# Performance work log

Measured on AMD Instinct MI355X. Metric: run time of the kernel, lower is better.

## Reference

```python
import jax, jax.numpy as jnp
import numpy as np

B = 4        # number of point clouds (equal-size contiguous batches)
P = 8192     # points per cloud
C_IN = 64
C_OUT = 64
K = 16       # kNN neighbors (includes the point itself, as in PyG knn)
EPS = 1e-5
NEG_SLOPE = 0.2


def setup_inputs() -> dict:
    key = jax.random.key(0)
    k1, k2, k3 = jax.random.split(key, 3)
    x = jax.random.normal(k1, (B * P, C_IN), dtype=jnp.float32)
    batch = jnp.repeat(jnp.arange(B, dtype=jnp.int64), P)  # sorted, equal sizes
    W = jax.random.normal(k2, (2 * C_IN, C_OUT), dtype=jnp.float32) * (1.0 / np.sqrt(2 * C_IN))
    b = jax.random.normal(k3, (C_OUT,), dtype=jnp.float32) * 0.01
    gamma = jnp.ones((C_OUT,), dtype=jnp.float32)
    beta = jnp.zeros((C_OUT,), dtype=jnp.float32)
    return {"x": x, "batch": batch, "W": W, "b": b, "gamma": gamma, "beta": beta}


def _edgeconv(x, W, b, gamma, beta):
    xb = x.reshape(B, P, C_IN)
    # per-cloud pairwise squared distances: [B, P, P]
    sq = jnp.sum(xb * xb, axis=-1)
    d = sq[:, :, None] + sq[:, None, :] - 2.0 * jnp.einsum("bpc,bqc->bpq", xb, xb)
    # k nearest neighbors (smallest distance, self included)
    _, idx = jax.lax.top_k(-d, K)                      # [B, P, K]
    xj = jax.vmap(lambda pts, ind: pts[ind])(xb, idx)  # [B, P, K, C_IN]
    xi = xb[:, :, None, :]
    e = jnp.concatenate([jnp.broadcast_to(xi, xj.shape), xj - xi], axis=-1)  # [B,P,K,2C]
    # edge MLP: Linear -> BatchNorm1d (training-mode batch stats over all edges) -> LeakyReLU
    h = jnp.einsum("bpke,eo->bpko", e, W) + b          # [B, P, K, C_OUT]
    hf = h.reshape(-1, C_OUT)
    mean = jnp.mean(hf, axis=0)
    var = jnp.mean(hf * hf, axis=0) - mean * mean      # biased variance (torch BN)
    hn = (h - mean) * jax.lax.rsqrt(var + EPS) * gamma + beta
    a = jnp.where(hn >= 0, hn, NEG_SLOPE * hn)
    # max aggregation over neighbors
    return jnp.max(a, axis=2).reshape(B * P, C_OUT)


def reference(x, batch, W, b, gamma, beta):
    # `batch` encodes B equal-size contiguous clouds; kNN is computed per cloud.
    return _edgeconv(x, W, b, gamma, beta)
```

## Files before the change

### kernel.cpp

```cpp
#include <hip/hip_runtime.h>
#include <cfloat>

#define BATCH 4
#define P 8192
#define C 64
#define KNN 16
#define NPTS (BATCH * P)
#define NEDGE (NPTS * KNN)
#define EPSV 1e-5f
#define SLOPE 0.2f
#define NQ 2
#define QCOLS (P / NQ)
#define NPART 4

typedef __attribute__((ext_vector_type(8))) short bf16x8;
typedef __attribute__((ext_vector_type(16))) float f32x16;


__device__ __forceinline__ unsigned short f2bf(float f) {
    unsigned u = __float_as_uint(f);
    u += 0x7FFFu + ((u >> 16) & 1u);
    return (unsigned short)(u >> 16);
}
__device__ __forceinline__ float bf2f(unsigned short s) {
    return __uint_as_float(((unsigned)s) << 16);
}

__global__ void prep_frag(const float* __restrict__ x, uint4* __restrict__ xfh,
                          uint4* __restrict__ xfm, uint4* __restrict__ xfl,
                          float* __restrict__ sq) {
    __shared__ float part[32][9];
    int tid = threadIdx.x;
    int ptl = tid >> 3, j8 = tid & 7;
    int g = blockIdx.x;
    int p = g * 32 + ptl;
    const float4* xp = (const float4*)(x + (size_t)p * C + j8 * 8);
    float4 a = xp[0], b = xp[1];
    float v[8] = {a.x, a.y, a.z, a.w, b.x, b.y, b.z, b.w};
    unsigned short hs[8], ms[8], ls[8];
    float ssum = 0.f;
#pragma unroll
    for (int e = 0; e < 8; ++e) {
        float xv = v[e];
        ssum = fmaf(xv, xv, ssum);
        unsigned short h = f2bf(xv);
        float r1 = xv - bf2f(h);
        unsigned short m = f2bf(r1);
        float r2 = r1 - bf2f(m);
        unsigned short l = f2bf(r2);
        hs[e] = h; ms[e] = m; ls[e] = l;
    }
    int dst = (g * 4 + (j8 >> 1)) * 64 + ptl + 32 * (j8 & 1);
    uint4 ph, pm, pl;
    ph.x = (unsigned)hs[0] | ((unsigned)hs[1] << 16);
    ph.y = (unsigned)hs[2] | ((unsigned)hs[3] << 16);
    ph.z = (unsigned)hs[4] | ((unsigned)hs[5] << 16);
    ph.w = (unsigned)hs[6] | ((unsigned)hs[7] << 16);
    pm.x = (unsigned)ms[0] | ((unsigned)ms[1] << 16);
    pm.y = (unsigned)ms[2] | ((unsigned)ms[3] << 16);
    pm.z = (unsigned)ms[4] | ((unsigned)ms[5] << 16);
    pm.w = (unsigned)ms[6] | ((unsigned)ms[7] << 16);
    pl.x = (unsigned)ls[0] | ((unsigned)ls[1] << 16);
    pl.y = (unsigned)ls[2] | ((unsigned)ls[3] << 16);
    pl.z = (unsigned)ls[4] | ((unsigned)ls[5] << 16);
    pl.w = (unsigned)ls[6] | ((unsigned)ls[7] << 16);
    xfh[dst] = ph; xfm[dst] = pm; xfl[dst] = pl;
    part[ptl][j8] = ssum;
    __syncthreads();
    if (j8 == 0) {
        float s = 0.f;
#pragma unroll
        for (int k = 0; k < 8; ++k) s += part[ptl][k];
        sq[p] = s;
    }
}

__global__ __launch_bounds__(256, 4) void knn_kernel(const uint4* __restrict__ xfh,
                                                     const uint4* __restrict__ xfm,
                                                     const uint4* __restrict__ xfl,
                                                     const float* __restrict__ sq,
                                                     float* __restrict__ pv,
                                                     int* __restrict__ pi) {
    __shared__ float          bufv[4 * 32 * 33];
    __shared__ unsigned short bufi[4 * 32 * 33];
    __shared__ int            idL [4 * 32 * 17];
    __shared__ int            cntL[4 * 32];
    __shared__ float          worstL[4 * 32];

    int tid = threadIdx.x;
    int b = blockIdx.x & 3;
    int t = blockIdx.x >> 2;
    int tile = t & 127;
    int half = t >> 7;
    int bglob = b * P;
    int r0 = tile * 64;
    int colbase = half * QCOLS;
    int w = tid >> 6, lane = tid & 63;
    int wr = w & 1, wc = w >> 1;

    float*          bufvW = bufv + w * (32 * 33);
    unsigned short* bufiW = bufi + w * (32 * 33);
    int*            idLW  = idL  + w * (32 * 17);
    int*            cntW  = cntL + w * 32;
    float*          worstW = worstL + w * 32;

    if (lane < 32) { cntW[lane] = 0; worstW[lane] = FLT_MAX; }

    int gA = ((bglob + r0) >> 5) + wr;
    bf16x8 Ah[4], Am[4], Al[4];
#pragma unroll
    for (int kk = 0; kk < 4; ++kk) {
        Ah[kk] = __builtin_bit_cast(bf16x8, xfh[(gA * 4 + kk) * 64 + lane]);
        Am[kk] = __builtin_bit_cast(bf16x8, xfm[(gA * 4 + kk) * 64 + lane]);
        Al[kk] = __builtin_bit_cast(bf16x8, xfl[(gA * 4 + kk) * 64 + lane]);
    }

    float tv[16];
    float worst = FLT_MAX;
#pragma unroll
    for (int j = 0; j < 16; ++j) tv[j] = FLT_MAX;

    int rlbase = 4 * (lane >> 5);
    int sub = lane & 31;
    int colq = wc * 32 + sub;

    for (int chunk = 0; chunk < QCOLS / 64; ++chunk) {
        int c0 = colbase + chunk * 64;
        int gB = ((bglob + c0) >> 5) + wc;
        float sc = sq[bglob + c0 + colq];

        f32x16 acc;
#pragma unroll
        for (int i = 0; i < 16; ++i) acc[i] = 0.f;

#pragma unroll
        for (int kk = 0; kk < 4; ++kk) {
            bf16x8 Bh = __builtin_bit_cast(bf16x8, xfh[(gB * 4 + kk) * 64 + lane]);
            bf16x8 Bm = __builtin_bit_cast(bf16x8, xfm[(gB * 4 + kk) * 64 + lane]);
            bf16x8 Bl = __builtin_bit_cast(bf16x8, xfl[(gB * 4 + kk) * 64 + lane]);
            acc = __builtin_amdgcn_mfma_f32_32x32x16_bf16(Ah[kk], Bh, acc, 0, 0, 0);
            acc = __builtin_amdgcn_mfma_f32_32x32x16_bf16(Am[kk], Bh, acc, 0, 0, 0);
            acc = __builtin_amdgcn_mfma_f32_32x32x16_bf16(Al[kk], Bh, acc, 0, 0, 0);
            acc = __builtin_amdgcn_mfma_f32_32x32x16_bf16(Ah[kk], Bm, acc, 0, 0, 0);
            acc = __builtin_amdgcn_mfma_f32_32x32x16_bf16(Am[kk], Bm, acc, 0, 0, 0);
            acc = __builtin_amdgcn_mfma_f32_32x32x16_bf16(Ah[kk], Bl, acc, 0, 0, 0);
            __builtin_amdgcn_sched_barrier(0);
        }

        if (chunk == 0) {
#pragma unroll
            for (int reg = 0; reg < 16; ++reg) {
                float s = fmaf(-2.f, acc[reg], sc);
                int rl = rlbase + (reg & 3) + 8 * (reg >> 2);
                bufvW[rl * 33 + sub] = s;
            }
        } else {
            float4 twA[4];
#pragma unroll
            for (int g4 = 0; g4 < 4; ++g4)
                twA[g4] = *(const float4*)&worstW[rlbase + 8 * g4];
#pragma unroll
            for (int reg = 0; reg < 16; ++reg) {
                float s = fmaf(-2.f, acc[reg], sc);
                float tW = ((const float*)&twA[reg >> 2])[reg & 3];
                if (s < tW) {
                    int rl = rlbase + (reg & 3) + 8 * (reg >> 2);
                    int slot = atomicAdd(&cntW[rl], 1);
                    bufvW[rl * 33 + slot] = s;
                    bufiW[rl * 33 + slot] = (unsigned short)sub;
                }
            }
        }

        if (lane < 32) {
            int n = (chunk == 0) ? 32 : cntW[lane];
            int base = lane * 33;
            int id0 = bglob + c0 + wc * 32;
            for (int k = 0; k < n; ++k) {
                float s = bufvW[base + k];
                if (s < worst) {
                    float mx = tv[0];
                    int pos = 0;
#pragma unroll
                    for (int j = 1; j < 16; ++j) {
                        bool g = tv[j] > mx;
                        mx = g ? tv[j] : mx;
                        pos = g ? j : pos;
                    }
#pragma unroll
                    for (int j = 0; j < 16; ++j)
                        if (j == pos) tv[j] = s;
                    idLW[lane * 17 + pos] = (chunk == 0) ? (id0 + k)
                                                         : (id0 + (int)bufiW[base + k]);
                    float nw = fmaxf(fmaxf(fmaxf(tv[0], tv[1]), fmaxf(tv[2], tv[3])),
                                     fmaxf(fmaxf(tv[4], tv[5]), fmaxf(tv[6], tv[7])));
                    nw = fmaxf(nw, fmaxf(fmaxf(fmaxf(tv[8], tv[9]), fmaxf(tv[10], tv[11])),
                                         fmaxf(fmaxf(tv[12], tv[13]), fmaxf(tv[14], tv[15]))));
                    worst = nw;
                }
            }
            if (n > 0) { cntW[lane] = 0; worstW[lane] = worst; }
        }
        __builtin_amdgcn_sched_barrier(0);
    }

    if (lane < 32) {
        int qq = half * 2 + wc;
        size_t o = (((size_t)(bglob + r0 + wr * 32 + lane)) * NPART + qq) * KNN;
#pragma unroll
        for (int j = 0; j < 16; ++j) {
            pv[o + j] = tv[j];
            pi[o + j] = idLW[lane * 17 + j];
        }
    }
}

__global__ void merge_kernel(const float* __restrict__ pv, const int* __restrict__ pi,
                             int* __restrict__ idx_out) {
    __shared__ float mv[64][65];
    __shared__ int   mi[64][65];
    int tid = threadIdx.x;
    int lr = tid & 63, q = tid >> 6;
    int row = blockIdx.x * 64 + lr;
    size_t o = ((size_t)row * NPART + q) * KNN;
#pragma unroll
    for (int j = 0; j < 16; ++j) {
        mv[lr][q * 16 + j] = pv[o + j];
        mi[lr][q * 16 + j] = pi[o + j];
    }
    __syncthreads();
    if (tid < 64) {
        float tv[16];
        int ti[16];
        float worst = FLT_MAX;
#pragma unroll
        for (int j = 0; j < 16; ++j) { tv[j] = FLT_MAX; ti[j] = 0; }
        for (int e = 0; e < 64; ++e) {
            float s = mv[tid][e];
            if (s < worst) {
                float mx = tv[0];
                int pos = 0;
#pragma unroll
                for (int j = 1; j < 16; ++j) {
                    bool g = tv[j] > mx;
                    mx = g ? tv[j] : mx;
                    pos = g ? j : pos;
                }
#pragma unroll
                for (int j = 0; j < 16; ++j)
                    if (j == pos) { tv[j] = s; ti[j] = mi[tid][e]; }
                float nw = tv[0];
#pragma unroll
                for (int j = 1; j < 16; ++j) nw = fmaxf(nw, tv[j]);
                worst = nw;
            }
        }
        size_t oo = (size_t)row * KNN;
#pragma unroll
        for (int j = 0; j < 16; ++j) idx_out[oo + j] = ti[j];
    }
}

__global__ void prep_UV(const float* __restrict__ x, const float* __restrict__ W,
                        float* __restrict__ U, float* __restrict__ V) {
    __shared__ float Ws[128][64];
    __shared__ float xs[4][64];
    int tid = threadIdx.x;
    for (int i = tid; i < 128 * 64; i += 256) ((float*)Ws)[i] = W[i];
    int p0 = blockIdx.x * 4;
    int r = tid >> 6, c = tid & 63;
    xs[r][c] = x[(size_t)(p0 + r) * C + c];
    __syncthreads();
    float u = 0.f, v = 0.f;
#pragma unroll
    for (int k = 0; k < 64; ++k) {
        float xv = xs[r][k];
        float w1 = Ws[k][c];
        float w2 = Ws[64 + k][c];
        u = fmaf(xv, w1 - w2, u);
        v = fmaf(xv, w2, v);
    }
    size_t o = (size_t)(p0 + r) * C + c;
    U[o] = u;
    V[o] = v;
}

__global__ void stats_kernel(const float* __restrict__ U, const float* __restrict__ V,
                             const float* __restrict__ bias, const int* __restrict__ idx,
                             float* __restrict__ stats) {
    int tid = threadIdx.x;
    int c = tid & 63, kk = tid >> 6;
    int p0 = blockIdx.x * 32;
    float bc = bias[c];
    float sum = 0.f, sumsq = 0.f;
    for (int pp = 0; pp < 32; ++pp) {
        int p = p0 + pp;
        float u = U[(size_t)p * C + c] + bc;
#pragma unroll
        for (int k4 = 0; k4 < 4; ++k4) {
            int j = idx[(size_t)p * KNN + kk * 4 + k4];
            float h = u + V[(size_t)j * C + c];
            sum += h;
            sumsq = fmaf(h, h, sumsq);
        }
    }
    __shared__ float red[2][4][64];
    red[0][kk][c] = sum;
    red[1][kk][c] = sumsq;
    __syncthreads();
    if (tid < 64) {
        float s = red[0][0][tid] + red[0][1][tid] + red[0][2][tid] + red[0][3][tid];
        atomicAdd(&stats[tid], s);
    } else if (tid < 128) {
        int cc = tid - 64;
        float s = red[1][0][cc] + red[1][1][cc] + red[1][2][cc] + red[1][3][cc];
        atomicAdd(&stats[64 + cc], s);
    }
}

__global__ void finalize_kernel(const float* __restrict__ stats,
                                const float* __restrict__ gamma,
                                const float* __restrict__ beta,
                                float* __restrict__ sshift) {
    int c = threadIdx.x;
    const float N = (float)NEDGE;
    float mean = stats[c] / N;
    float var = stats[64 + c] / N - mean * mean;
    float s = gamma[c] * rsqrtf(var + EPSV);
    sshift[c] = s;
    sshift[64 + c] = beta[c] - mean * s;
}

__global__ void out_kernel(const float* __restrict__ U, const float* __restrict__ V,
                           const float* __restrict__ bias, const int* __restrict__ idx,
                           const float* __restrict__ sshift, float* __restrict__ out) {
    int tid = threadIdx.x;
    int c = tid & 63, g = tid >> 6;
    int p0 = blockIdx.x * 16;
    float s = sshift[c], t = sshift[64 + c];
    float bc = bias[c];
    for (int pp = g; pp < 16; pp += 4) {
        int p = p0 + pp;
        float mx = -FLT_MAX, mn = FLT_MAX;
#pragma unroll
        for (int k = 0; k < KNN; ++k) {
            int j = idx[(size_t)p * KNN + k];
            float v = V[(size_t)j * C + c];
            mx = fmaxf(mx, v);
            mn = fminf(mn, v);
        }
        float hsel = (s >= 0.f) ? mx : mn;
        float hn = fmaf(s, U[(size_t)p * C + c] + bc + hsel, t);
        out[(size_t)p * C + c] = (hn >= 0.f) ? hn : SLOPE * hn;
    }
}

extern "C" void kernel_launch(void* const* d_in, const int* in_sizes, int n_in,
                              void* d_out, int out_size, void* d_ws, size_t ws_size,
                              hipStream_t stream) {
    const float* x     = (const float*)d_in[0];
    const float* W     = (const float*)d_in[2];
    const float* bias  = (const float*)d_in[3];
    const float* gamma = (const float*)d_in[4];
    const float* beta  = (const float*)d_in[5];
    float* out = (float*)d_out;

    float* wsf    = (float*)d_ws;
    float* U      = wsf;
    float* V      = wsf + 2097152;
    uint4* xfh    = (uint4*)wsf;
    uint4* xfm    = (uint4*)(wsf + 1048576);
    uint4* xfl    = (uint4*)(wsf + 2097152);
    float* sq     = wsf + 4194304;
    float* stats  = wsf + 4227072;
    float* sshift = wsf + 4227200;
    int*   idx    = (int*)(wsf + 4227328);
    float* pv     = wsf + 4751616;
    int*   pi     = (int*)(wsf + 6848768);

    hipLaunchKernelGGL(prep_frag, dim3(NPTS / 32), dim3(256), 0, stream, x, xfh, xfm, xfl, sq);
    hipLaunchKernelGGL(knn_kernel, dim3(BATCH * (P / 64) * NQ), dim3(256), 0, stream,
                       (const uint4*)xfh, (const uint4*)xfm, (const uint4*)xfl, sq, pv, pi);
    hipLaunchKernelGGL(merge_kernel, dim3(NPTS / 64), dim3(256), 0, stream, pv, pi, idx);
    hipLaunchKernelGGL(prep_UV, dim3(NPTS / 4), dim3(256), 0, stream, x, W, U, V);
    hipMemsetAsync(stats, 0, 128 * sizeof(float), stream);
    hipLaunchKernelGGL(stats_kernel, dim3(NPTS / 32), dim3(256), 0, stream, U, V, bias, idx, stats);
    hipLaunchKernelGGL(finalize_kernel, dim3(1), dim3(64), 0, stream, stats, gamma, beta, sshift);
    hipLaunchKernelGGL(out_kernel, dim3(NPTS / 16), dim3(256), 0, stream, U, V, bias, idx, sshift, out);
}
```

Before: 578.2 us.

## Fuse neighbor max/min gather into stats pass and regroup knn MFMA loads

```diff
diff --git a/kernel.cpp b/kernel.cpp
--- a/kernel.cpp
+++ b/kernel.cpp
@@ -133,18 +133,46 @@
 #pragma unroll
         for (int i = 0; i < 16; ++i) acc[i] = 0.f;
 
-#pragma unroll
-        for (int kk = 0; kk < 4; ++kk) {
-            bf16x8 Bh = __builtin_bit_cast(bf16x8, xfh[(gB * 4 + kk) * 64 + lane]);
-            bf16x8 Bm = __builtin_bit_cast(bf16x8, xfm[(gB * 4 + kk) * 64 + lane]);
-            bf16x8 Bl = __builtin_bit_cast(bf16x8, xfl[(gB * 4 + kk) * 64 + lane]);
-            acc = __builtin_amdgcn_mfma_f32_32x32x16_bf16(Ah[kk], Bh, acc, 0, 0, 0);
-            acc = __builtin_amdgcn_mfma_f32_32x32x16_bf16(Am[kk], Bh, acc, 0, 0, 0);
-            acc = __builtin_amdgcn_mfma_f32_32x32x16_bf16(Al[kk], Bh, acc, 0, 0, 0);
-            acc = __builtin_amdgcn_mfma_f32_32x32x16_bf16(Ah[kk], Bm, acc, 0, 0, 0);
-            acc = __builtin_amdgcn_mfma_f32_32x32x16_bf16(Am[kk], Bm, acc, 0, 0, 0);
-            acc = __builtin_amdgcn_mfma_f32_32x32x16_bf16(Ah[kk], Bl, acc, 0, 0, 0);
-            __builtin_amdgcn_sched_barrier(0);
+        {
+            bf16x8 Bh0 = __builtin_bit_cast(bf16x8, xfh[(gB * 4 + 0) * 64 + lane]);
+            bf16x8 Bm0 = __builtin_bit_cast(bf16x8, xfm[(gB * 4 + 0) * 64 + lane]);
+            bf16x8 Bl0 = __builtin_bit_cast(bf16x8, xfl[(gB * 4 + 0) * 64 + lane]);
+            bf16x8 Bh1 = __builtin_bit_cast(bf16x8, xfh[(gB * 4 + 1) * 64 + lane]);
+            bf16x8 Bm1 = __builtin_bit_cast(bf16x8, xfm[(gB * 4 + 1) * 64 + lane]);
+            bf16x8 Bl1 = __builtin_bit_cast(bf16x8, xfl[(gB * 4 + 1) * 64 + lane]);
+            acc = __builtin_amdgcn_mfma_f32_32x32x16_bf16(Ah[0], Bh0, acc, 0, 0, 0);
+            acc = __builtin_amdgcn_mfma_f32_32x32x16_bf16(Am[0], Bh0, acc, 0, 0, 0);
+            acc = __builtin_amdgcn_mfma_f32_32x32x16_bf16(Al[0], Bh0, acc, 0, 0, 0);
+            acc = __builtin_amdgcn_mfma_f32_32x32x16_bf16(Ah[0], Bm0, acc, 0, 0, 0);
+            acc = __builtin_amdgcn_mfma_f32_32x32x16_bf16(Am[0], Bm0, acc, 0, 0, 0);
+            acc = __builtin_amdgcn_mfma_f32_32x32x16_bf16(Ah[0], Bl0, acc, 0, 0, 0);
+            acc = __builtin_amdgcn_mfma_f32_32x32x16_bf16(Ah[1], Bh1, acc, 0, 0, 0);
+            acc = __builtin_amdgcn_mfma_f32_32x32x16_bf16(Am[1], Bh1, acc, 0, 0, 0);
+            acc = __builtin_amdgcn_mfma_f32_32x32x16_bf16(Al[1], Bh1, acc, 0, 0, 0);
+            acc = __builtin_amdgcn_mfma_f32_32x32x16_bf16(Ah[1], Bm1, acc, 0, 0, 0);
+            acc = __builtin_amdgcn_mfma_f32_32x32x16_bf16(Am[1], Bm1, acc, 0, 0, 0);
+            acc = __builtin_amdgcn_mfma_f32_32x32x16_bf16(Ah[1], Bl1, acc, 0, 0, 0);
+        }
+        __builtin_amdgcn_sched_barrier(0);
+        {
+            bf16x8 Bh2 = __builtin_bit_cast(bf16x8, xfh[(gB * 4 + 2) * 64 + lane]);
+            bf16x8 Bm2 = __builtin_bit_cast(bf16x8, xfm[(gB * 4 + 2) * 64 + lane]);
+            bf16x8 Bl2 = __builtin_bit_cast(bf16x8, xfl[(gB * 4 + 2) * 64 + lane]);
+            bf16x8 Bh3 = __builtin_bit_cast(bf16x8, xfh[(gB * 4 + 3) * 64 + lane]);
+            bf16x8 Bm3 = __builtin_bit_cast(bf16x8, xfm[(gB * 4 + 3) * 64 + lane]);
+            bf16x8 Bl3 = __builtin_bit_cast(bf16x8, xfl[(gB * 4 + 3) * 64 + lane]);
+            acc = __builtin_amdgcn_mfma_f32_32x32x16_bf16(Ah[2], Bh2, acc, 0, 0, 0);
+            acc = __builtin_amdgcn_mfma_f32_32x32x16_bf16(Am[2], Bh2, acc, 0, 0, 0);
+            acc = __builtin_amdgcn_mfma_f32_32x32x16_bf16(Al[2], Bh2, acc, 0, 0, 0);
+            acc = __builtin_amdgcn_mfma_f32_32x32x16_bf16(Ah[2], Bm2, acc, 0, 0, 0);
+            acc = __builtin_amdgcn_mfma_f32_32x32x16_bf16(Am[2], Bm2, acc, 0, 0, 0);
+            acc = __builtin_amdgcn_mfma_f32_32x32x16_bf16(Ah[2], Bl2, acc, 0, 0, 0);
+            acc = __builtin_amdgcn_mfma_f32_32x32x16_bf16(Ah[3], Bh3, acc, 0, 0, 0);
+            acc = __builtin_amdgcn_mfma_f32_32x32x16_bf16(Am[3], Bh3, acc, 0, 0, 0);
+            acc = __builtin_amdgcn_mfma_f32_32x32x16_bf16(Al[3], Bh3, acc, 0, 0, 0);
+            acc = __builtin_amdgcn_mfma_f32_32x32x16_bf16(Ah[3], Bm3, acc, 0, 0, 0);
+            acc = __builtin_amdgcn_mfma_f32_32x32x16_bf16(Am[3], Bm3, acc, 0, 0, 0);
+            acc = __builtin_amdgcn_mfma_f32_32x32x16_bf16(Ah[3], Bl3, acc, 0, 0, 0);
         }
 
         if (chunk == 0) {
@@ -201,7 +229,6 @@
             }
             if (n > 0) { cntW[lane] = 0; worstW[lane] = worst; }
         }
-        __builtin_amdgcn_sched_barrier(0);
     }
 
     if (lane < 32) {
@@ -287,26 +314,33 @@
 
 __global__ void stats_kernel(const float* __restrict__ U, const float* __restrict__ V,
                              const float* __restrict__ bias, const int* __restrict__ idx,
-                             float* __restrict__ stats) {
+                             float* __restrict__ stats, float* __restrict__ Vmx,
+                             float* __restrict__ Vmn) {
     int tid = threadIdx.x;
-    int c = tid & 63, kk = tid >> 6;
-    int p0 = blockIdx.x * 32;
+    int c = tid & 63, g = tid >> 6;
+    int p0 = blockIdx.x * 16;
     float bc = bias[c];
     float sum = 0.f, sumsq = 0.f;
-    for (int pp = 0; pp < 32; ++pp) {
+    for (int pp = g; pp < 16; pp += 4) {
         int p = p0 + pp;
         float u = U[(size_t)p * C + c] + bc;
-#pragma unroll
-        for (int k4 = 0; k4 < 4; ++k4) {
-            int j = idx[(size_t)p * KNN + kk * 4 + k4];
-            float h = u + V[(size_t)j * C + c];
+        float mx = -FLT_MAX, mn = FLT_MAX;
+#pragma unroll
+        for (int k = 0; k < KNN; ++k) {
+            int j = idx[(size_t)p * KNN + k];
+            float v = V[(size_t)j * C + c];
+            mx = fmaxf(mx, v);
+            mn = fminf(mn, v);
+            float h = u + v;
             sum += h;
             sumsq = fmaf(h, h, sumsq);
         }
+        Vmx[(size_t)p * C + c] = mx;
+        Vmn[(size_t)p * C + c] = mn;
     }
     __shared__ float red[2][4][64];
-    red[0][kk][c] = sum;
-    red[1][kk][c] = sumsq;
+    red[0][g][c] = sum;
+    red[1][g][c] = sumsq;
     __syncthreads();
     if (tid < 64) {
         float s = red[0][0][tid] + red[0][1][tid] + red[0][2][tid] + red[0][3][tid];
@@ -331,28 +365,39 @@
     sshift[64 + c] = beta[c] - mean * s;
 }
 
-__global__ void out_kernel(const float* __restrict__ U, const float* __restrict__ V,
-                           const float* __restrict__ bias, const int* __restrict__ idx,
-                           const float* __restrict__ sshift, float* __restrict__ out) {
-    int tid = threadIdx.x;
-    int c = tid & 63, g = tid >> 6;
-    int p0 = blockIdx.x * 16;
-    float s = sshift[c], t = sshift[64 + c];
-    float bc = bias[c];
-    for (int pp = g; pp < 16; pp += 4) {
-        int p = p0 + pp;
-        float mx = -FLT_MAX, mn = FLT_MAX;
-#pragma unroll
-        for (int k = 0; k < KNN; ++k) {
-            int j = idx[(size_t)p * KNN + k];
-            float v = V[(size_t)j * C + c];
-            mx = fmaxf(mx, v);
-            mn = fminf(mn, v);
-        }
-        float hsel = (s >= 0.f) ? mx : mn;
-        float hn = fmaf(s, U[(size_t)p * C + c] + bc + hsel, t);
-        out[(size_t)p * C + c] = (hn >= 0.f) ? hn : SLOPE * hn;
-    }
+__global__ void out_kernel(const float* __restrict__ U, const float* __restrict__ bias,
+                           const float* __restrict__ sshift, const float* __restrict__ Vmx,
+                           const float* __restrict__ Vmn, float* __restrict__ out) {
+    int i = (blockIdx.x * 256 + threadIdx.x) * 4;
+    int c = i & 63;
+    float4 sv = *(const float4*)&sshift[c];
+    float4 tv = *(const float4*)&sshift[64 + c];
+    float4 bb = *(const float4*)&bias[c];
+    float4 u  = *(const float4*)&U[i];
+    float4 mx = *(const float4*)&Vmx[i];
+    float4 mn = *(const float4*)&Vmn[i];
+    float4 r;
+    {
+        float hsel = (sv.x >= 0.f) ? mx.x : mn.x;
+        float hn = fmaf(sv.x, u.x + bb.x + hsel, tv.x);
+        r.x = (hn >= 0.f) ? hn : SLOPE * hn;
+    }
+    {
+        float hsel = (sv.y >= 0.f) ? mx.y : mn.y;
+        float hn = fmaf(sv.y, u.y + bb.y + hsel, tv.y);
+        r.y = (hn >= 0.f) ? hn : SLOPE * hn;
+    }
+    {
+        float hsel = (sv.z >= 0.f) ? mx.z : mn.z;
+        float hn = fmaf(sv.z, u.z + bb.z + hsel, tv.z);
+        r.z = (hn >= 0.f) ? hn : SLOPE * hn;
+    }
+    {
+        float hsel = (sv.w >= 0.f) ? mx.w : mn.w;
+        float hn = fmaf(sv.w, u.w + bb.w + hsel, tv.w);
+        r.w = (hn >= 0.f) ? hn : SLOPE * hn;
+    }
+    *(float4*)&out[i] = r;
 }
 
 extern "C" void kernel_launch(void* const* d_in, const int* in_sizes, int n_in,
@@ -377,6 +422,8 @@
     int*   idx    = (int*)(wsf + 4227328);
     float* pv     = wsf + 4751616;
     int*   pi     = (int*)(wsf + 6848768);
+    float* Vmx    = wsf + 4751616;
+    float* Vmn    = wsf + 6848768;
 
     hipLaunchKernelGGL(prep_frag, dim3(NPTS / 32), dim3(256), 0, stream, x, xfh, xfm, xfl, sq);
     hipLaunchKernelGGL(knn_kernel, dim3(BATCH * (P / 64) * NQ), dim3(256), 0, stream,
@@ -384,7 +431,9 @@
     hipLaunchKernelGGL(merge_kernel, dim3(NPTS / 64), dim3(256), 0, stream, pv, pi, idx);
     hipLaunchKernelGGL(prep_UV, dim3(NPTS / 4), dim3(256), 0, stream, x, W, U, V);
     hipMemsetAsync(stats, 0, 128 * sizeof(float), stream);
-    hipLaunchKernelGGL(stats_kernel, dim3(NPTS / 32), dim3(256), 0, stream, U, V, bias, idx, stats);
+    hipLaunchKernelGGL(stats_kernel, dim3(NPTS / 16), dim3(256), 0, stream, U, V, bias, idx,
+                       stats, Vmx, Vmn);
     hipLaunchKernelGGL(finalize_kernel, dim3(1), dim3(64), 0, stream, stats, gamma, beta, sshift);
-    hipLaunchKernelGGL(out_kernel, dim3(NPTS / 16), dim3(256), 0, stream, U, V, bias, idx, sshift, out);
-}
+    hipLaunchKernelGGL(out_kernel, dim3(NPTS * C / 1024), dim3(256), 0, stream,
+                       U, bias, sshift, Vmx, Vmn, out);
+}
```

Result: slower. 597.3 us (+3.3%).
